# Performance work log

Hardware: AMD Instinct MI355X
Metric: run time of the kernel (lower is better)

The kernel has to match this reference:

```python
import jax, jax.numpy as jnp
import numpy as np

EXTEND_EPS = 0.04
DEPTH_MIN = 0.1
EDGE_MAX = 0.1
B, C, H, W = 8, 4, 512, 512


def _make_lin(n):
    lin = jnp.linspace(0.5, n - 0.5, n, dtype=jnp.float32)
    return lin.at[-1].add(EXTEND_EPS)


def _mesh_structure(h, w):
    # static triangle topology of the image grid: (2*(h-1)*(w-1), 3) int32
    x, y = jnp.meshgrid(jnp.arange(w, dtype=jnp.int32), jnp.arange(h, dtype=jnp.int32), indexing='xy')
    pts = y[:-1, :-1] * w + x[:-1, :-1]
    lower = jnp.stack([pts, pts + w, pts + w + 1], axis=2).reshape(-1, 3)
    upper = jnp.stack([pts, pts + w + 1, pts + 1], axis=2).reshape(-1, 3)
    return jnp.concatenate([lower, upper], axis=0)


def _unproject(attr_d, c2w_int, c2w_ext):
    # attr_d: (H, W, 4) = RGB + depth; returns flattened verts (HW,3), attrs (HW,3), depth (HW,)
    h, w, _ = attr_d.shape
    x, y = jnp.meshgrid(_make_lin(w), _make_lin(h), indexing='xy')
    z = attr_d[..., -1]
    a = attr_d[..., :-1]
    # boundary extrapolation by extend_eps (all three updates read disjoint, unmodified entries)
    a = a.at[-1, :-1].add((a[-1, :-1] - a[-2, :-1]) * EXTEND_EPS)
    a = a.at[:-1, -1].add((a[:-1, -1] - a[:-1, -2]) * EXTEND_EPS)
    a = a.at[-1, -1].add((a[-1, -1] - a[-2, -2]) * EXTEND_EPS)
    v = jnp.stack([x * z, y * z, z], axis=-1)              # (H,W,3) camera rays * depth
    v = jnp.einsum('ij,hwj->hwi', c2w_int, v)              # intrinsics
    v = jnp.concatenate([v, jnp.ones_like(v[..., :1])], axis=-1)
    v = jnp.einsum('ij,hwj->hwi', c2w_ext, v)              # (H,W,3) world coords
    return v.reshape(-1, 3), a.reshape(-1, 3), z.reshape(-1)


def _mesh_one(attr_d, c2w_int, c2w_ext, faces):
    v, a, d = _unproject(attr_d, c2w_int, c2w_ext)
    msk0 = jnp.all(d[faces] > DEPTH_MIN, axis=1)           # valid-depth faces
    tri = v[faces]                                         # (F,3,3) gather
    e = tri - jnp.roll(tri, -1, axis=1)                    # edges v0-v1, v1-v2, v2-v0
    edge_len = jnp.sqrt(jnp.sum(e * e, axis=-1))           # (F,3)
    msk1 = jnp.all(edge_len < EDGE_MAX, axis=1)
    return v, a, edge_len, msk0 & msk1


def reference(attr_d, c2w_int, c2w_ext):
    # attr_d: (B, 4, H, W)
    ad = jnp.transpose(attr_d, (0, 2, 3, 1))               # (B,H,W,4)
    faces = _mesh_structure(H, W)
    v, a, edge_len, msk = jax.vmap(lambda x, ki, ke: _mesh_one(x, ki, ke, faces))(ad, c2w_int, c2w_ext)
    return v, a, edge_len, msk


def setup_inputs() -> dict:
    key = jax.random.key(0)
    k1, k2, k3 = jax.random.split(key, 3)
    attr_d = jax.random.uniform(k1, (B, C, H, W), dtype=jnp.float32)
    c2w_int = jax.random.normal(k2, (B, 3, 3), dtype=jnp.float32)
    c2w_ext = jax.random.normal(k3, (B, 3, 4), dtype=jnp.float32)
    return {'attr_d': attr_d, 'c2w_int': c2w_int, 'c2w_ext': c2w_ext}
```

## Files before the change

kernel.cpp:

```cpp
#include <hip/hip_runtime.h>

#define HH 512
#define WW 512
#define NB 8
constexpr int   NPIX = HH * WW;
constexpr int   FH   = (HH - 1) * (WW - 1);
constexpr int   NF   = 2 * FH;
constexpr float EPS       = 0.04f;
constexpr float DEPTH_MIN = 0.1f;
constexpr float EDGE_MAX  = 0.1f;

__device__ __forceinline__ float elen(float ax, float ay, float az,
                                      float bx, float by, float bz) {
    float dx = ax - bx, dy = ay - by, dz = az - bz;
    return sqrtf(dx * dx + dy * dy + dz * dz);
}

__device__ __forceinline__ float nbr(float cur, float nxt, int lane) {
    float t = (lane == 0) ? nxt : cur;
    return __shfl(t, (lane + 1) & 63);
}

__device__ __forceinline__ void wcopy(const float* __restrict__ s,
                                      float* __restrict__ d, int n, int lane) {
    int head = (int)(((16u - (unsigned)((uintptr_t)d & 15u)) & 15u) >> 2);
    if (head > n) head = n;
    if (lane < head) d[lane] = s[lane];
    int n4 = (n - head) >> 2;
    const float* s2 = s + head;
    float* d2 = d + head;
    for (int i = lane; i < n4; i += 64) {
        float4 t = make_float4(s2[4*i], s2[4*i+1], s2[4*i+2], s2[4*i+3]);
        *(float4*)(d2 + 4*i) = t;
    }
    int done = n4 << 2;
    int rem  = n - head - done;
    if (lane < rem) d2[done + lane] = s2[done + lane];
}

__global__ void __launch_bounds__(64)
fused_kernel(const float* __restrict__ attr_d,
             const float* __restrict__ c2w_int,
             const float* __restrict__ c2w_ext,
             float* __restrict__ out_v,
             float* __restrict__ out_a,
             float* __restrict__ out_e,
             float* __restrict__ out_m) {
    __shared__ float lds[1536];
    const int lane = threadIdx.x;
    const int task = blockIdx.x;
    const int b    = task / 511;
    const int y    = task - b * 511;

    const float* base  = attr_d + (size_t)b * 4 * NPIX;
    const float* zrow0 = base + 3 * NPIX + (size_t)y * WW;
    const float* zrow1 = zrow0 + WW;

    float z0[8], z1[8], a0[3][8];
#pragma unroll
    for (int j = 0; j < 8; ++j) {
        z0[j] = zrow0[lane + 64*j];
        z1[j] = zrow1[lane + 64*j];
    }
#pragma unroll
    for (int c = 0; c < 3; ++c) {
        const float* ar = base + c * NPIX + (size_t)y * WW;
#pragma unroll
        for (int j = 0; j < 8; ++j) a0[c][j] = ar[lane + 64*j];
    }

#pragma unroll
    for (int c = 0; c < 3; ++c) {
        float left = __shfl_up(a0[c][7], 1);
        if (lane == 63) a0[c][7] += (a0[c][7] - left) * EPS;
    }

    const float* K = c2w_int + b * 9;
    const float* E = c2w_ext + b * 12;
    const float K0=K[0],K1=K[1],K2=K[2],K3=K[3],K4=K[4],K5=K[5],K6=K[6],K7=K[7],K8=K[8];
    const float E0=E[0],E1=E[1],E2=E[2],E3=E[3],E4=E[4],E5=E[5],
                E6=E[6],E7=E[7],E8=E[8],E9=E[9],E10=E[10],E11=E[11];

    const float yc0 = (float)y + 0.5f;
    const float yc1 = (y + 1 == HH - 1) ? ((float)HH - 0.5f + EPS)
                                        : ((float)(y + 1) + 0.5f);

    float v0x[8],v0y[8],v0z[8], v1x[8],v1y[8],v1z[8];
#pragma unroll
    for (int j = 0; j < 8; ++j) {
        int col = lane + 64*j;
        float xc = (col == WW - 1) ? ((float)WW - 0.5f + EPS) : ((float)col + 0.5f);
        {
            float p0 = xc*z0[j], p1 = yc0*z0[j], p2 = z0[j];
            float vi0 = K0*p0 + K1*p1 + K2*p2;
            float vi1 = K3*p0 + K4*p1 + K5*p2;
            float vi2 = K6*p0 + K7*p1 + K8*p2;
            v0x[j] = E0*vi0 + E1*vi1 + E2 *vi2 + E3;
            v0y[j] = E4*vi0 + E5*vi1 + E6 *vi2 + E7;
            v0z[j] = E8*vi0 + E9*vi1 + E10*vi2 + E11;
        }
        {
            float p0 = xc*z1[j], p1 = yc1*z1[j], p2 = z1[j];
            float vi0 = K0*p0 + K1*p1 + K2*p2;
            float vi1 = K3*p0 + K4*p1 + K5*p2;
            float vi2 = K6*p0 + K7*p1 + K8*p2;
            v1x[j] = E0*vi0 + E1*vi1 + E2 *vi2 + E3;
            v1y[j] = E4*vi0 + E5*vi1 + E6 *vi2 + E7;
            v1z[j] = E8*vi0 + E9*vi1 + E10*vi2 + E11;
        }
    }

    size_t rb = ((size_t)b * NPIX + (size_t)y * WW) * 3;
#pragma unroll
    for (int j = 0; j < 8; ++j) {
        int c3 = (lane + 64*j) * 3;
        lds[c3] = v0x[j]; lds[c3+1] = v0y[j]; lds[c3+2] = v0z[j];
    }
    wcopy(lds, out_v + rb, 1536, lane);
#pragma unroll
    for (int j = 0; j < 8; ++j) {
        int c3 = (lane + 64*j) * 3;
        lds[c3] = a0[0][j]; lds[c3+1] = a0[1][j]; lds[c3+2] = a0[2][j];
    }
    wcopy(lds, out_a + rb, 1536, lane);

    float vert[8];
#pragma unroll
    for (int j = 0; j < 8; ++j)
        vert[j] = elen(v0x[j],v0y[j],v0z[j], v1x[j],v1y[j],v1z[j]);

    float bot[8], diag[8], top[8], vertn[8];
    size_t mlo = (size_t)b * NF + (size_t)y * (WW-1);
    size_t mup = mlo + FH;
#pragma unroll
    for (int j = 0; j < 8; ++j) {
        const int jn = (j < 7) ? j + 1 : j;
        float n0x = nbr(v0x[j], v0x[jn], lane);
        float n0y = nbr(v0y[j], v0y[jn], lane);
        float n0z = nbr(v0z[j], v0z[jn], lane);
        float n1x = nbr(v1x[j], v1x[jn], lane);
        float n1y = nbr(v1y[j], v1y[jn], lane);
        float n1z = nbr(v1z[j], v1z[jn], lane);
        float zt1 = nbr(z0[j],  z0[jn],  lane);
        float zb1 = nbr(z1[j],  z1[jn],  lane);
        vertn[j]  = nbr(vert[j], vert[jn], lane);

        top[j]  = elen(v0x[j],v0y[j],v0z[j], n0x,n0y,n0z);
        bot[j]  = elen(v1x[j],v1y[j],v1z[j], n1x,n1y,n1z);
        diag[j] = elen(v0x[j],v0y[j],v0z[j], n1x,n1y,n1z);

        bool ml = (z0[j] > DEPTH_MIN) & (z1[j] > DEPTH_MIN) & (zb1 > DEPTH_MIN) &
                  (vert[j] < EDGE_MAX) & (bot[j] < EDGE_MAX) & (diag[j] < EDGE_MAX);
        bool mu = (z0[j] > DEPTH_MIN) & (zb1 > DEPTH_MIN) & (zt1 > DEPTH_MIN) &
                  (diag[j] < EDGE_MAX) & (vertn[j] < EDGE_MAX) & (top[j] < EDGE_MAX);

        int col = lane + 64*j;
        if (col < WW - 1) {
            out_m[mlo + col] = ml ? 1.0f : 0.0f;
            out_m[mup + col] = mu ? 1.0f : 0.0f;
        }
    }

    size_t elo = mlo * 3;
#pragma unroll
    for (int j = 0; j < 8; ++j) {
        int col = lane + 64*j;
        if (col < WW - 1) {
            int c3 = col * 3;
            lds[c3] = vert[j]; lds[c3+1] = bot[j]; lds[c3+2] = diag[j];
        }
    }
    wcopy(lds, out_e + elo, 1533, lane);
#pragma unroll
    for (int j = 0; j < 8; ++j) {
        int col = lane + 64*j;
        if (col < WW - 1) {
            int c3 = col * 3;
            lds[c3] = diag[j]; lds[c3+1] = vertn[j]; lds[c3+2] = top[j];
        }
    }
    wcopy(lds, out_e + elo + (size_t)FH * 3, 1533, lane);

    if (y == HH - 2) {
        float a1[3][8];
#pragma unroll
        for (int c = 0; c < 3; ++c) {
            const float* ar = base + c * NPIX + (size_t)(HH-1) * WW;
#pragma unroll
            for (int j = 0; j < 8; ++j) a1[c][j] = ar[lane + 64*j];
            float dl = __shfl_up(a0[c][7], 1);
#pragma unroll
            for (int j = 0; j < 8; ++j) {
                int col = lane + 64*j;
                if (col < WW - 1) a1[c][j] += (a1[c][j] - a0[c][j]) * EPS;
            }
            if (lane == 63) a1[c][7] += (a1[c][7] - dl) * EPS;
        }
        size_t rb1 = ((size_t)b * NPIX + (size_t)(HH-1) * WW) * 3;
#pragma unroll
        for (int j = 0; j < 8; ++j) {
            int c3 = (lane + 64*j) * 3;
            lds[c3] = v1x[j]; lds[c3+1] = v1y[j]; lds[c3+2] = v1z[j];
        }
        wcopy(lds, out_v + rb1, 1536, lane);
#pragma unroll
        for (int j = 0; j < 8; ++j) {
            int c3 = (lane + 64*j) * 3;
            lds[c3] = a1[0][j]; lds[c3+1] = a1[1][j]; lds[c3+2] = a1[2][j];
        }
        wcopy(lds, out_a + rb1, 1536, lane);
    }
}

extern "C" void kernel_launch(void* const* d_in, const int* in_sizes, int n_in,
                              void* d_out, int out_size, void* d_ws, size_t ws_size,
                              hipStream_t stream) {
    const float* attr_d  = (const float*)d_in[0];
    const float* c2w_int = (const float*)d_in[1];
    const float* c2w_ext = (const float*)d_in[2];

    float* out   = (float*)d_out;
    float* out_v = out;
    float* out_a = out + (size_t)NB * NPIX * 3;
    float* out_e = out + (size_t)2 * NB * NPIX * 3;
    float* out_m = out_e + (size_t)NB * NF * 3;

    int tasks = NB * (HH - 1);
    fused_kernel<<<tasks, 64, 0, stream>>>(attr_d, c2w_int, c2w_ext,
                                           out_v, out_a, out_e, out_m);
}
```

Measured before the change: 28.28 us.

## Vectorize loads and LDS staging with 4-column-per-lane layout

Each lane now owns 4 consecutive columns rather than strided ones, so input rows load as float4 and the AoS staging into LDS uses float4 stores. Horizontal neighbours come from registers, which leaves only one cross-lane shuffle per group. Mask outputs are staged through LDS and written with the aligned vector copy instead of scalar stores. A second LDS buffer lets both edge halves be staged before copying. The cost is extra LDS and a likely rise in register pressure from the larger per-lane working set.

```diff
diff --git a/kernel.cpp b/kernel.cpp
--- a/kernel.cpp
+++ b/kernel.cpp
@@ -14,11 +14,6 @@
                                       float bx, float by, float bz) {
     float dx = ax - bx, dy = ay - by, dz = az - bz;
     return sqrtf(dx * dx + dy * dy + dz * dz);
-}
-
-__device__ __forceinline__ float nbr(float cur, float nxt, int lane) {
-    float t = (lane == 0) ? nxt : cur;
-    return __shfl(t, (lane + 1) & 63);
 }
 
 __device__ __forceinline__ void wcopy(const float* __restrict__ s,
@@ -46,33 +41,38 @@
              float* __restrict__ out_a,
              float* __restrict__ out_e,
              float* __restrict__ out_m) {
-    __shared__ float lds[1536];
+    __shared__ float ldsA[1536];
+    __shared__ float ldsB[1536];
     const int lane = threadIdx.x;
     const int task = blockIdx.x;
     const int b    = task / 511;
     const int y    = task - b * 511;
 
-    const float* base  = attr_d + (size_t)b * 4 * NPIX;
-    const float* zrow0 = base + 3 * NPIX + (size_t)y * WW;
-    const float* zrow1 = zrow0 + WW;
-
-    float z0[8], z1[8], a0[3][8];
-#pragma unroll
-    for (int j = 0; j < 8; ++j) {
-        z0[j] = zrow0[lane + 64*j];
-        z1[j] = zrow1[lane + 64*j];
-    }
-#pragma unroll
-    for (int c = 0; c < 3; ++c) {
-        const float* ar = base + c * NPIX + (size_t)y * WW;
-#pragma unroll
-        for (int j = 0; j < 8; ++j) a0[c][j] = ar[lane + 64*j];
-    }
-
-#pragma unroll
-    for (int c = 0; c < 3; ++c) {
-        float left = __shfl_up(a0[c][7], 1);
-        if (lane == 63) a0[c][7] += (a0[c][7] - left) * EPS;
+    const float* base = attr_d + (size_t)b * 4 * NPIX;
+    const float* zr0  = base + 3 * NPIX + (size_t)y * WW;
+
+    float z0[2][4], z1[2][4], a0[3][2][4];
+#pragma unroll
+    for (int g = 0; g < 2; ++g) {
+        int c = (g << 8) + (lane << 2);
+        float4 t0 = *(const float4*)(zr0 + c);
+        float4 t1 = *(const float4*)(zr0 + WW + c);
+        z0[g][0]=t0.x; z0[g][1]=t0.y; z0[g][2]=t0.z; z0[g][3]=t0.w;
+        z1[g][0]=t1.x; z1[g][1]=t1.y; z1[g][2]=t1.z; z1[g][3]=t1.w;
+    }
+#pragma unroll
+    for (int ch = 0; ch < 3; ++ch) {
+        const float* ar = base + ch * NPIX + (size_t)y * WW;
+#pragma unroll
+        for (int g = 0; g < 2; ++g) {
+            float4 t = *(const float4*)(ar + (g << 8) + (lane << 2));
+            a0[ch][g][0]=t.x; a0[ch][g][1]=t.y; a0[ch][g][2]=t.z; a0[ch][g][3]=t.w;
+        }
+    }
+    if (lane == 63) {
+#pragma unroll
+        for (int ch = 0; ch < 3; ++ch)
+            a0[ch][1][3] += (a0[ch][1][3] - a0[ch][1][2]) * EPS;
     }
 
     const float* K = c2w_int + b * 9;
@@ -85,131 +85,163 @@
     const float yc1 = (y + 1 == HH - 1) ? ((float)HH - 0.5f + EPS)
                                         : ((float)(y + 1) + 0.5f);
 
-    float v0x[8],v0y[8],v0z[8], v1x[8],v1y[8],v1z[8];
-#pragma unroll
-    for (int j = 0; j < 8; ++j) {
-        int col = lane + 64*j;
-        float xc = (col == WW - 1) ? ((float)WW - 0.5f + EPS) : ((float)col + 0.5f);
-        {
-            float p0 = xc*z0[j], p1 = yc0*z0[j], p2 = z0[j];
-            float vi0 = K0*p0 + K1*p1 + K2*p2;
-            float vi1 = K3*p0 + K4*p1 + K5*p2;
-            float vi2 = K6*p0 + K7*p1 + K8*p2;
-            v0x[j] = E0*vi0 + E1*vi1 + E2 *vi2 + E3;
-            v0y[j] = E4*vi0 + E5*vi1 + E6 *vi2 + E7;
-            v0z[j] = E8*vi0 + E9*vi1 + E10*vi2 + E11;
-        }
-        {
-            float p0 = xc*z1[j], p1 = yc1*z1[j], p2 = z1[j];
-            float vi0 = K0*p0 + K1*p1 + K2*p2;
-            float vi1 = K3*p0 + K4*p1 + K5*p2;
-            float vi2 = K6*p0 + K7*p1 + K8*p2;
-            v1x[j] = E0*vi0 + E1*vi1 + E2 *vi2 + E3;
-            v1y[j] = E4*vi0 + E5*vi1 + E6 *vi2 + E7;
-            v1z[j] = E8*vi0 + E9*vi1 + E10*vi2 + E11;
-        }
-    }
+    float v0x[2][4], v0y[2][4], v0z[2][4], v1x[2][4], v1y[2][4], v1z[2][4];
+#pragma unroll
+    for (int g = 0; g < 2; ++g) {
+#pragma unroll
+        for (int j = 0; j < 4; ++j) {
+            int col = (g << 8) + (lane << 2) + j;
+            float xc = (col == WW - 1) ? ((float)WW - 0.5f + EPS)
+                                       : ((float)col + 0.5f);
+            {
+                float zz = z0[g][j];
+                float p0 = xc*zz, p1 = yc0*zz;
+                float vi0 = K0*p0 + K1*p1 + K2*zz;
+                float vi1 = K3*p0 + K4*p1 + K5*zz;
+                float vi2 = K6*p0 + K7*p1 + K8*zz;
+                v0x[g][j] = E0*vi0 + E1*vi1 + E2 *vi2 + E3;
+                v0y[g][j] = E4*vi0 + E5*vi1 + E6 *vi2 + E7;
+                v0z[g][j] = E8*vi0 + E9*vi1 + E10*vi2 + E11;
+            }
+            {
+                float zz = z1[g][j];
+                float p0 = xc*zz, p1 = yc1*zz;
+                float vi0 = K0*p0 + K1*p1 + K2*zz;
+                float vi1 = K3*p0 + K4*p1 + K5*zz;
+                float vi2 = K6*p0 + K7*p1 + K8*zz;
+                v1x[g][j] = E0*vi0 + E1*vi1 + E2 *vi2 + E3;
+                v1y[g][j] = E4*vi0 + E5*vi1 + E6 *vi2 + E7;
+                v1z[g][j] = E8*vi0 + E9*vi1 + E10*vi2 + E11;
+            }
+        }
+    }
+
+    float4* A4 = (float4*)ldsA;
+    float4* B4 = (float4*)ldsB;
 
     size_t rb = ((size_t)b * NPIX + (size_t)y * WW) * 3;
 #pragma unroll
-    for (int j = 0; j < 8; ++j) {
-        int c3 = (lane + 64*j) * 3;
-        lds[c3] = v0x[j]; lds[c3+1] = v0y[j]; lds[c3+2] = v0z[j];
-    }
-    wcopy(lds, out_v + rb, 1536, lane);
-#pragma unroll
-    for (int j = 0; j < 8; ++j) {
-        int c3 = (lane + 64*j) * 3;
-        lds[c3] = a0[0][j]; lds[c3+1] = a0[1][j]; lds[c3+2] = a0[2][j];
-    }
-    wcopy(lds, out_a + rb, 1536, lane);
-
-    float vert[8];
-#pragma unroll
-    for (int j = 0; j < 8; ++j)
-        vert[j] = elen(v0x[j],v0y[j],v0z[j], v1x[j],v1y[j],v1z[j]);
-
-    float bot[8], diag[8], top[8], vertn[8];
-    size_t mlo = (size_t)b * NF + (size_t)y * (WW-1);
+    for (int g = 0; g < 2; ++g) {
+        int o = 192*g + 3*lane;
+        A4[o]   = make_float4(v0x[g][0], v0y[g][0], v0z[g][0], v0x[g][1]);
+        A4[o+1] = make_float4(v0y[g][1], v0z[g][1], v0x[g][2], v0y[g][2]);
+        A4[o+2] = make_float4(v0z[g][2], v0x[g][3], v0y[g][3], v0z[g][3]);
+    }
+    wcopy(ldsA, out_v + rb, 1536, lane);
+#pragma unroll
+    for (int g = 0; g < 2; ++g) {
+        int o = 192*g + 3*lane;
+        A4[o]   = make_float4(a0[0][g][0], a0[1][g][0], a0[2][g][0], a0[0][g][1]);
+        A4[o+1] = make_float4(a0[1][g][1], a0[2][g][1], a0[0][g][2], a0[1][g][2]);
+        A4[o+2] = make_float4(a0[2][g][2], a0[0][g][3], a0[1][g][3], a0[2][g][3]);
+    }
+    wcopy(ldsA, out_a + rb, 1536, lane);
+
+    if (y == HH - 2) {
+        float a1[3][2][4];
+#pragma unroll
+        for (int ch = 0; ch < 3; ++ch) {
+            const float* ar = base + ch * NPIX + (size_t)(HH-1) * WW;
+#pragma unroll
+            for (int g = 0; g < 2; ++g) {
+                float4 t = *(const float4*)(ar + (g << 8) + (lane << 2));
+                a1[ch][g][0]=t.x; a1[ch][g][1]=t.y; a1[ch][g][2]=t.z; a1[ch][g][3]=t.w;
+            }
+#pragma unroll
+            for (int g = 0; g < 2; ++g)
+#pragma unroll
+            for (int j = 0; j < 4; ++j) {
+                int col = (g << 8) + (lane << 2) + j;
+                if (col < WW - 1)
+                    a1[ch][g][j] += (a1[ch][g][j] - a0[ch][g][j]) * EPS;
+            }
+            if (lane == 63)
+                a1[ch][1][3] += (a1[ch][1][3] - a0[ch][1][2]) * EPS;
+        }
+        size_t rb1 = ((size_t)b * NPIX + (size_t)(HH-1) * WW) * 3;
+#pragma unroll
+        for (int g = 0; g < 2; ++g) {
+            int o = 192*g + 3*lane;
+            A4[o]   = make_float4(v1x[g][0], v1y[g][0], v1z[g][0], v1x[g][1]);
+            A4[o+1] = make_float4(v1y[g][1], v1z[g][1], v1x[g][2], v1y[g][2]);
+            A4[o+2] = make_float4(v1z[g][2], v1x[g][3], v1y[g][3], v1z[g][3]);
+        }
+        wcopy(ldsA, out_v + rb1, 1536, lane);
+#pragma unroll
+        for (int g = 0; g < 2; ++g) {
+            int o = 192*g + 3*lane;
+            A4[o]   = make_float4(a1[0][g][0], a1[1][g][0], a1[2][g][0], a1[0][g][1]);
+            A4[o+1] = make_float4(a1[1][g][1], a1[2][g][1], a1[0][g][2], a1[1][g][2]);
+            A4[o+2] = make_float4(a1[2][g][2], a1[0][g][3], a1[1][g][3], a1[2][g][3]);
+        }
+        wcopy(ldsA, out_a + rb1, 1536, lane);
+    }
+
+    float vert[2][4];
+#pragma unroll
+    for (int g = 0; g < 2; ++g)
+#pragma unroll
+    for (int j = 0; j < 4; ++j)
+        vert[g][j] = elen(v0x[g][j],v0y[g][j],v0z[g][j],
+                          v1x[g][j],v1y[g][j],v1z[g][j]);
+
+    float n0x[2],n0y[2],n0z[2],n1x[2],n1y[2],n1z[2],nz0[2],nz1[2],nvt[2];
+#pragma unroll
+    for (int g = 0; g < 2; ++g) {
+        int src = (lane + 1) & 63;
+#define NBR(dst, arr) { float s_ = (g == 0 && lane == 0) ? arr[1][0] : arr[g][0]; \
+                        dst[g] = __shfl(s_, src); }
+        NBR(n0x, v0x) NBR(n0y, v0y) NBR(n0z, v0z)
+        NBR(n1x, v1x) NBR(n1y, v1y) NBR(n1z, v1z)
+        NBR(nz0, z0)  NBR(nz1, z1)  NBR(nvt, vert)
+#undef NBR
+    }
+
+    float mlv[2][4], muv[2][4];
+#pragma unroll
+    for (int g = 0; g < 2; ++g) {
+        float tp[4], bt[4], dg[4], vn[4];
+#pragma unroll
+        for (int j = 0; j < 4; ++j) {
+            float px0 = (j<3)? v0x[g][j+1] : n0x[g];
+            float py0 = (j<3)? v0y[g][j+1] : n0y[g];
+            float pz0 = (j<3)? v0z[g][j+1] : n0z[g];
+            float px1 = (j<3)? v1x[g][j+1] : n1x[g];
+            float py1 = (j<3)? v1y[g][j+1] : n1y[g];
+            float pz1 = (j<3)? v1z[g][j+1] : n1z[g];
+            float zt1 = (j<3)? z0[g][j+1]  : nz0[g];
+            float zb1 = (j<3)? z1[g][j+1]  : nz1[g];
+            vn[j]     = (j<3)? vert[g][j+1] : nvt[g];
+            tp[j] = elen(v0x[g][j],v0y[g][j],v0z[g][j], px0,py0,pz0);
+            bt[j] = elen(v1x[g][j],v1y[g][j],v1z[g][j], px1,py1,pz1);
+            dg[j] = elen(v0x[g][j],v0y[g][j],v0z[g][j], px1,py1,pz1);
+            bool ml = (z0[g][j] > DEPTH_MIN) & (z1[g][j] > DEPTH_MIN) & (zb1 > DEPTH_MIN) &
+                      (vert[g][j] < EDGE_MAX) & (bt[j] < EDGE_MAX) & (dg[j] < EDGE_MAX);
+            bool mu = (z0[g][j] > DEPTH_MIN) & (zb1 > DEPTH_MIN) & (zt1 > DEPTH_MIN) &
+                      (dg[j] < EDGE_MAX) & (vn[j] < EDGE_MAX) & (tp[j] < EDGE_MAX);
+            mlv[g][j] = ml ? 1.0f : 0.0f;
+            muv[g][j] = mu ? 1.0f : 0.0f;
+        }
+        int o = 192*g + 3*lane;
+        A4[o]   = make_float4(vert[g][0], bt[0], dg[0], vert[g][1]);
+        A4[o+1] = make_float4(bt[1], dg[1], vert[g][2], bt[2]);
+        A4[o+2] = make_float4(dg[2], vert[g][3], bt[3], dg[3]);
+        B4[o]   = make_float4(dg[0], vn[0], tp[0], dg[1]);
+        B4[o+1] = make_float4(vn[1], tp[1], dg[2], vn[2]);
+        B4[o+2] = make_float4(tp[2], dg[3], vn[3], tp[3]);
+    }
+    size_t mlo = (size_t)b * NF + (size_t)y * (WW - 1);
     size_t mup = mlo + FH;
-#pragma unroll
-    for (int j = 0; j < 8; ++j) {
-        const int jn = (j < 7) ? j + 1 : j;
-        float n0x = nbr(v0x[j], v0x[jn], lane);
-        float n0y = nbr(v0y[j], v0y[jn], lane);
-        float n0z = nbr(v0z[j], v0z[jn], lane);
-        float n1x = nbr(v1x[j], v1x[jn], lane);
-        float n1y = nbr(v1y[j], v1y[jn], lane);
-        float n1z = nbr(v1z[j], v1z[jn], lane);
-        float zt1 = nbr(z0[j],  z0[jn],  lane);
-        float zb1 = nbr(z1[j],  z1[jn],  lane);
-        vertn[j]  = nbr(vert[j], vert[jn], lane);
-
-        top[j]  = elen(v0x[j],v0y[j],v0z[j], n0x,n0y,n0z);
-        bot[j]  = elen(v1x[j],v1y[j],v1z[j], n1x,n1y,n1z);
-        diag[j] = elen(v0x[j],v0y[j],v0z[j], n1x,n1y,n1z);
-
-        bool ml = (z0[j] > DEPTH_MIN) & (z1[j] > DEPTH_MIN) & (zb1 > DEPTH_MIN) &
-                  (vert[j] < EDGE_MAX) & (bot[j] < EDGE_MAX) & (diag[j] < EDGE_MAX);
-        bool mu = (z0[j] > DEPTH_MIN) & (zb1 > DEPTH_MIN) & (zt1 > DEPTH_MIN) &
-                  (diag[j] < EDGE_MAX) & (vertn[j] < EDGE_MAX) & (top[j] < EDGE_MAX);
-
-        int col = lane + 64*j;
-        if (col < WW - 1) {
-            out_m[mlo + col] = ml ? 1.0f : 0.0f;
-            out_m[mup + col] = mu ? 1.0f : 0.0f;
-        }
-    }
-
-    size_t elo = mlo * 3;
-#pragma unroll
-    for (int j = 0; j < 8; ++j) {
-        int col = lane + 64*j;
-        if (col < WW - 1) {
-            int c3 = col * 3;
-            lds[c3] = vert[j]; lds[c3+1] = bot[j]; lds[c3+2] = diag[j];
-        }
-    }
-    wcopy(lds, out_e + elo, 1533, lane);
-#pragma unroll
-    for (int j = 0; j < 8; ++j) {
-        int col = lane + 64*j;
-        if (col < WW - 1) {
-            int c3 = col * 3;
-            lds[c3] = diag[j]; lds[c3+1] = vertn[j]; lds[c3+2] = top[j];
-        }
-    }
-    wcopy(lds, out_e + elo + (size_t)FH * 3, 1533, lane);
-
-    if (y == HH - 2) {
-        float a1[3][8];
-#pragma unroll
-        for (int c = 0; c < 3; ++c) {
-            const float* ar = base + c * NPIX + (size_t)(HH-1) * WW;
-#pragma unroll
-            for (int j = 0; j < 8; ++j) a1[c][j] = ar[lane + 64*j];
-            float dl = __shfl_up(a0[c][7], 1);
-#pragma unroll
-            for (int j = 0; j < 8; ++j) {
-                int col = lane + 64*j;
-                if (col < WW - 1) a1[c][j] += (a1[c][j] - a0[c][j]) * EPS;
-            }
-            if (lane == 63) a1[c][7] += (a1[c][7] - dl) * EPS;
-        }
-        size_t rb1 = ((size_t)b * NPIX + (size_t)(HH-1) * WW) * 3;
-#pragma unroll
-        for (int j = 0; j < 8; ++j) {
-            int c3 = (lane + 64*j) * 3;
-            lds[c3] = v1x[j]; lds[c3+1] = v1y[j]; lds[c3+2] = v1z[j];
-        }
-        wcopy(lds, out_v + rb1, 1536, lane);
-#pragma unroll
-        for (int j = 0; j < 8; ++j) {
-            int c3 = (lane + 64*j) * 3;
-            lds[c3] = a1[0][j]; lds[c3+1] = a1[1][j]; lds[c3+2] = a1[2][j];
-        }
-        wcopy(lds, out_a + rb1, 1536, lane);
-    }
+    wcopy(ldsA, out_e + mlo * 3, 1533, lane);
+    wcopy(ldsB, out_e + mup * 3, 1533, lane);
+
+#pragma unroll
+    for (int g = 0; g < 2; ++g) {
+        A4[(g << 6) + lane]       = make_float4(mlv[g][0], mlv[g][1], mlv[g][2], mlv[g][3]);
+        A4[128 + (g << 6) + lane] = make_float4(muv[g][0], muv[g][1], muv[g][2], muv[g][3]);
+    }
+    wcopy(ldsA,       out_m + mlo, 511, lane);
+    wcopy(ldsA + 512, out_m + mup, 511, lane);
 }
 
 extern "C" void kernel_launch(void* const* d_in, const int* in_sizes, int n_in,
```

Result: slower. 30.83 us (+9.0%).
